# Optimization experiments

Measured on AMD Instinct MI355X. Metric: run time of the kernel, lower is better.

Reference implementation:

```python
import jax, jax.numpy as jnp
import numpy as np

D_MODEL = 2048
N_HEAD = 32
N_KV_HEAD = 8
HEAD_DIM = D_MODEL // N_HEAD  # 64
N_REP = N_HEAD // N_KV_HEAD   # 4
B, T = 2, 2048


def setup_inputs() -> dict:
    key = jax.random.key(0)
    ks = jax.random.split(key, 5)
    s = 0.02
    return {
        "x": jax.random.normal(ks[0], (B, T, D_MODEL), dtype=jnp.float32),
        "Wq": jax.random.normal(ks[1], (D_MODEL, N_HEAD * HEAD_DIM), dtype=jnp.float32) * s,
        "Wk": jax.random.normal(ks[2], (D_MODEL, N_KV_HEAD * HEAD_DIM), dtype=jnp.float32) * s,
        "Wv": jax.random.normal(ks[3], (D_MODEL, N_KV_HEAD * HEAD_DIM), dtype=jnp.float32) * s,
        "Wo": jax.random.normal(ks[4], (N_HEAD * HEAD_DIM, D_MODEL), dtype=jnp.float32) * s,
        "mask": 1,
    }


def _rope_tables(t_len, dim, dtype):
    inv_freq = 1.0 / (10000.0 ** (jnp.arange(0, dim, 2, dtype=jnp.float32) / dim))
    freqs = jnp.arange(t_len, dtype=jnp.float32)[:, None] * inv_freq[None, :]  # [T, dim/2]
    return jnp.cos(freqs).astype(dtype), jnp.sin(freqs).astype(dtype)


def _apply_rope(x, cos, sin):
    # x: [B, H, T, D]; cos/sin: [T, D/2]; half-concat layout as in source
    x1, x2 = x[..., ::2], x[..., 1::2]
    return jnp.concatenate([x1 * cos - x2 * sin, x1 * sin + x2 * cos], axis=-1)


def reference(x, Wq, Wk, Wv, Wo, mask):
    b, t, c = x.shape
    q = (x @ Wq).reshape(b, t, N_HEAD, HEAD_DIM).transpose(0, 2, 1, 3)      # [B,H,T,D]
    k = (x @ Wk).reshape(b, t, N_KV_HEAD, HEAD_DIM).transpose(0, 2, 1, 3)   # [B,Hkv,T,D]
    v = (x @ Wv).reshape(b, t, N_KV_HEAD, HEAD_DIM).transpose(0, 2, 1, 3)
    cos, sin = _rope_tables(t, HEAD_DIM, x.dtype)
    q = _apply_rope(q, cos, sin)
    k = _apply_rope(k, cos, sin)
    k = jnp.repeat(k, N_REP, axis=1)  # [B,H,T,D]
    v = jnp.repeat(v, N_REP, axis=1)
    scale = 1.0 / np.sqrt(HEAD_DIM)
    scores = jnp.einsum('bhtd,bhsd->bhts', q, k) * scale  # [B,H,T,T]
    if mask:
        causal = jnp.tril(jnp.ones((t, t), dtype=bool))
        scores = jnp.where(causal, scores, jnp.float32(-jnp.inf).astype(scores.dtype))
    weights = jax.nn.softmax(scores, axis=-1)
    out = jnp.einsum('bhts,bhsd->bhtd', weights, v)        # [B,H,T,D]
    out = out.transpose(0, 2, 1, 3).reshape(b, t, c)
    return out @ Wo
```

## Files before the change

kernel.cpp:

```cpp
#include <hip/hip_runtime.h>
#include <stdint.h>

#define D_MODEL 2048
#define N_HEAD 32
#define N_KV_HEAD 8
#define HEAD_DIM 64
#define BATCH 2
#define SEQ 2048
#define ROWS (BATCH*SEQ)
#define QKV_N 3072
#define SCL2F 0.18033688011112042f

typedef __attribute__((ext_vector_type(4))) float f32x4;
typedef __attribute__((ext_vector_type(8))) short bf16x8;

__device__ __forceinline__ float bflo(unsigned u){ return __uint_as_float(u << 16); }
__device__ __forceinline__ float bfhi(unsigned u){ return __uint_as_float(u & 0xFFFF0000u); }
__device__ __forceinline__ unsigned f2bf(float f){
  unsigned u = __float_as_uint(f);
  u += 0x7FFFu + ((u >> 16) & 1u);
  return u >> 16;
}
__device__ __forceinline__ unsigned cvtpk(float a, float b){
  unsigned r;
  asm("v_cvt_pk_bf16_f32 %0, %1, %2" : "=v"(r) : "v"(a), "v"(b));
  return r;
}

__device__ __forceinline__ void async_copy16(const void* g, void* lds){
  __builtin_amdgcn_global_load_lds(
      (const __attribute__((address_space(1))) void*)g,
      (__attribute__((address_space(3))) void*)lds, 16, 0, 0);
}

__global__ __launch_bounds__(256) void k_cvt_bf16(const float* __restrict__ in,
                                                  unsigned short* __restrict__ out, int n4){
  int i = blockIdx.x*256 + threadIdx.x;
  if (i >= n4) return;
  float4 v = ((const float4*)in)[i];
  unsigned lo = f2bf(v.x) | (f2bf(v.y) << 16);
  unsigned hi = f2bf(v.z) | (f2bf(v.w) << 16);
  ((uint2*)out)[i] = make_uint2(lo, hi);
}

__global__ __launch_bounds__(256) void k_transpose_all(const float* __restrict__ Wq,
                                                       const float* __restrict__ Wk,
                                                       const float* __restrict__ Wv,
                                                       const float* __restrict__ Wo,
                                                       unsigned short* __restrict__ Wqkvt,
                                                       unsigned short* __restrict__ Wot){
  const int bid = blockIdx.x;
  const float* W; unsigned short* Wt; int N; int rel;
  if (bid < 1024)      { W = Wq; Wt = Wqkvt;                         N = 2048; rel = bid; }
  else if (bid < 1280) { W = Wk; Wt = Wqkvt + (size_t)2048*D_MODEL;  N = 512;  rel = bid - 1024; }
  else if (bid < 1536) { W = Wv; Wt = Wqkvt + (size_t)2560*D_MODEL;  N = 512;  rel = bid - 1280; }
  else                 { W = Wo; Wt = Wot;                           N = 2048; rel = bid - 1536; }
  __shared__ float tile[64][65];
  const int ntn = N >> 6;
  const int tk = rel / ntn, tn = rel % ntn;
  const int tid = threadIdx.x;
  #pragma unroll
  for (int i = 0; i < 4; ++i) {
    int idx4 = tid + 256*i;
    int r = idx4 >> 4;
    int c4 = idx4 & 15;
    float4 v = *(const float4*)(W + (size_t)(tk*64 + r)*N + tn*64 + c4*4);
    tile[r][c4*4+0] = v.x; tile[r][c4*4+1] = v.y;
    tile[r][c4*4+2] = v.z; tile[r][c4*4+3] = v.w;
  }
  __syncthreads();
  #pragma unroll
  for (int i = 0; i < 8; ++i) {
    int o2 = tid + 256*i;
    int n  = o2 >> 5;
    int k2 = o2 & 31;
    unsigned lo = f2bf(tile[k2*2+0][n]);
    unsigned hi = f2bf(tile[k2*2+1][n]);
    *(unsigned*)(Wt + (size_t)(tn*64 + n)*D_MODEL + tk*64 + k2*2) = lo | (hi << 16);
  }
}

__global__ __launch_bounds__(256) void k_rope_tables(float* __restrict__ ct, float* __restrict__ st){
  int gid = blockIdx.x*256 + threadIdx.x;
  int t = gid >> 5, d = gid & 31;
  float inv = exp2f(-13.287712379549449f * ((float)d * (1.0f/32.0f)));
  float a = (float)t * inv;
  ct[gid] = cosf(a);
  st[gid] = sinf(a);
}

__global__ __launch_bounds__(256) void k_rope_apply(unsigned short* __restrict__ X,
                                                    const float* __restrict__ ct,
                                                    const float* __restrict__ st,
                                                    int nheads, int stride, float scale){
  int gid = blockIdx.x*256 + threadIdx.x;
  int row = gid / nheads;
  int h = gid - row*nheads;
  int t = row & (SEQ-1);
  unsigned* p = (unsigned*)(X + (size_t)row*stride + h*HEAD_DIM);
  float o1[32], o2[32];
  #pragma unroll
  for (int d = 0; d < 32; ++d) {
    unsigned u = p[d];
    float x1 = bflo(u), x2 = bfhi(u);
    float c = ct[t*32+d], s = st[t*32+d];
    o1[d] = (x1*c - x2*s)*scale;
    o2[d] = (x1*s + x2*c)*scale;
  }
  #pragma unroll
  for (int i = 0; i < 16; ++i) {
    p[i]    = f2bf(o1[2*i]) | (f2bf(o1[2*i+1]) << 16);
    p[16+i] = f2bf(o2[2*i]) | (f2bf(o2[2*i+1]) << 16);
  }
}

template<typename OUT_T>
__global__ __launch_bounds__(256) void k_gemm_bt(const unsigned short* __restrict__ A,
                                                 const unsigned short* __restrict__ Bt,
                                                 OUT_T* __restrict__ C,
                                                 int M, int N, int K){
  __shared__ unsigned short As[128*32];
  __shared__ unsigned short Bs[128*32];
  const int nbn = N >> 7;
  const int bm = blockIdx.x / nbn, bn = blockIdx.x % nbn;
  const int m0 = bm << 7, n0 = bn << 7;
  const int tid = threadIdx.x;
  const int wid = tid >> 6, lane = tid & 63;
  const int wr = wid >> 1, wc = wid & 1;

  f32x4 acc[4][4] = {};

  const int ldr = lane >> 2;
  const int ldc = (lane & 3) * 8;
  const int fr  = lane & 15;
  const int fk  = (lane >> 4) * 8;

  for (int k0 = 0; k0 < K; k0 += 32) {
    #pragma unroll
    for (int i = 0; i < 2; ++i) {
      int chunk = wid*2 + i;
      int row = chunk*16 + ldr;
      async_copy16(A  + (size_t)(m0+row)*K + k0 + ldc, (void*)(As + chunk*512));
      async_copy16(Bt + (size_t)(n0+row)*K + k0 + ldc, (void*)(Bs + chunk*512));
    }
    __syncthreads();
    bf16x8 a[4], b[4];
    #pragma unroll
    for (int m = 0; m < 4; ++m) a[m] = *(const bf16x8*)(As + (wr*64 + m*16 + fr)*32 + fk);
    #pragma unroll
    for (int n = 0; n < 4; ++n) b[n] = *(const bf16x8*)(Bs + (wc*64 + n*16 + fr)*32 + fk);
    #pragma unroll
    for (int m = 0; m < 4; ++m)
      #pragma unroll
      for (int n = 0; n < 4; ++n)
        acc[m][n] = __builtin_amdgcn_mfma_f32_16x16x32_bf16(a[m], b[n], acc[m][n], 0, 0, 0);
    __syncthreads();
  }

  const int crow = (lane >> 4) * 4, ccol = lane & 15;
  #pragma unroll
  for (int m = 0; m < 4; ++m){
    #pragma unroll
    for (int n = 0; n < 4; ++n){
      size_t base = (size_t)(m0 + wr*64 + m*16 + crow)*N + (n0 + wc*64 + n*16 + ccol);
      #pragma unroll
      for (int j = 0; j < 4; ++j){
        float v = acc[m][n][j];
        if constexpr (sizeof(OUT_T) == 2)
          ((unsigned short*)C)[base + (size_t)j*N] = (unsigned short)f2bf(v);
        else
          ((float*)C)[base + (size_t)j*N] = v;
      }
    }
  }
}

__global__ __launch_bounds__(256) void k_transpose_v(const unsigned short* __restrict__ Vsrc,
                                                     unsigned short* __restrict__ Vt, int stride){
  __shared__ __align__(16) unsigned short t[64*64];
  const int bk = blockIdx.x >> 5;
  const int st = blockIdx.x & 31;
  const int b = bk >> 3, kvh = bk & 7;
  const int tid = threadIdx.x;
  #pragma unroll
  for (int it = 0; it < 2; ++it) {
    int i = tid + 256*it;
    int s = i >> 3, c = i & 7;
    uint4 v = *(const uint4*)(Vsrc + (size_t)(b*SEQ + st*64 + s)*stride + kvh*HEAD_DIM + c*8);
    *(uint4*)(t + s*64 + ((c ^ (s&7))*8)) = v;
  }
  __syncthreads();
  const int d = tid & 63;
  const int w = tid >> 6;
  #pragma unroll
  for (int it = 0; it < 2; ++it) {
    int seg = w + it*4;
    unsigned short tmp[8];
    #pragma unroll
    for (int k = 0; k < 8; ++k) {
      int s = seg*8 + k;
      tmp[k] = t[s*64 + (((d>>3) ^ (s&7))*8) + (d&7)];
    }
    *(uint4*)(Vt + ((size_t)bk*64 + d)*SEQ + st*64 + seg*8) = *(uint4*)tmp;
  }
}

__global__ __launch_bounds__(256) void k_attn_mfma(const unsigned short* __restrict__ Q,
                                                   const unsigned short* __restrict__ Kb,
                                                   const unsigned short* __restrict__ Vt,
                                                   unsigned short* __restrict__ O,
                                                   const int* __restrict__ maskp,
                                                   const float* __restrict__ ct,
                                                   const float* __restrict__ st){
  __shared__ __align__(16) char smem[32768];
  char* Vsm = smem + 16384;
  const int orig = blockIdx.x;
  const int bid = (orig & 7)*128 + (orig >> 3);
  const int jj = bid & 15;
  const int h  = (bid >> 4) & 31;
  const int b  = bid >> 9;
  const int kvh = h >> 2;
  const int tid = threadIdx.x;
  const int wid = tid >> 6, lane = tid & 63;
  const int q_ = lane & 15, g = lane >> 4;
  char* Psm = smem + 24576 + wid*2048;
  const bool causal = (maskp[0] != 0);

  auto stageK = [&](int tile, int bufbase){
    const int s0s = tile*64;
    #pragma unroll
    for (int it = 0; it < 2; ++it) {
      int i = (wid*2+it)*64 + lane;
      int s = i >> 3, c = i & 7;
      async_copy16(Kb + (size_t)(b*SEQ + s0s + s)*QKV_N + kvh*HEAD_DIM + ((c ^ (s&7))*8),
                   smem + bufbase + (wid*2+it)*1024);
    }
  };
  auto stageV = [&](int tile){
    const int s0s = tile*64;
    #pragma unroll
    for (int it = 0; it < 2; ++it) {
      int i = (wid*2+it)*64 + lane;
      int s = i >> 3, c = i & 7;
      async_copy16(Vt + ((size_t)(b*N_KV_HEAD + kvh)*HEAD_DIM + s)*SEQ + s0s + ((c ^ (s&7))*8),
                   Vsm + (wid*2+it)*1024);
    }
  };

  for (int pass = 0; pass < 2; ++pass) {
    const int qt = pass ? jj : (31 - jj);
    const int q0 = qt*64;
    const int qg = q0 + 16*wid + q_;
    const int nt = causal ? (qt+1) : (SEQ/64);

    bf16x8 qf0, qf1;
    {
      const int trow = qg;
      const unsigned short* qsrc = Q + (size_t)(b*SEQ + trow)*QKV_N + h*HEAD_DIM + g*16;
      union { bf16x8 h; unsigned u[4]; } xa, xb;
      xa.h = *(const bf16x8*)(qsrc);
      xb.h = *(const bf16x8*)(qsrc + 8);
      const float4* cp = (const float4*)(ct + trow*32 + g*8);
      const float4* sp = (const float4*)(st + trow*32 + g*8);
      float4 c0 = cp[0], c1 = cp[1];
      float4 s0 = sp[0], s1 = sp[1];
      float cc[8] = {c0.x,c0.y,c0.z,c0.w,c1.x,c1.y,c1.z,c1.w};
      float ss[8] = {s0.x,s0.y,s0.z,s0.w,s1.x,s1.y,s1.z,s1.w};
      float e0[8], e1[8];
      #pragma unroll
      for (int e = 0; e < 8; ++e) {
        unsigned u = (e < 4) ? xa.u[e] : xb.u[e-4];
        float x1 = bflo(u), x2 = bfhi(u);
        float cs = cc[e]*SCL2F, sn = ss[e]*SCL2F;
        e0[e] = x1*cs - x2*sn;
        e1[e] = x1*sn + x2*cs;
      }
      union { unsigned u[4]; bf16x8 h; } p0, p1;
      #pragma unroll
      for (int m = 0; m < 4; ++m) {
        p0.u[m] = cvtpk(e0[2*m], e0[2*m+1]);
        p1.u[m] = cvtpk(e1[2*m], e1[2*m+1]);
      }
      qf0 = p0.h; qf1 = p1.h;
    }

    f32x4 acc[4] = {};
    float mrun = -1e30f, lrun = 0.f;

    stageK(0, 0);
    stageV(0);
    asm volatile("s_waitcnt vmcnt(0)" ::: "memory");
    __syncthreads();

    for (int t = 0; t < nt; ++t) {
      const int s0 = t*64;
      const int cur = t & 1;
      const char* Kbuf = smem + cur*8192;

      if (t+1 < nt) stageK(t+1, (cur^1)*8192);

      f32x4 sa[4];
      __builtin_amdgcn_s_setprio(1);
      #pragma unroll
      for (int f = 0; f < 4; ++f) {
        const char* kb = Kbuf + (16*f + q_)*128;
        bf16x8 a0 = *(const bf16x8*)(kb + ((g ^ (q_&7))*16));
        bf16x8 a1 = *(const bf16x8*)(kb + (((g+4) ^ (q_&7))*16));
        f32x4 z = {};
        z = __builtin_amdgcn_mfma_f32_16x16x32_bf16(a0, qf0, z, 0, 0, 0);
        z = __builtin_amdgcn_mfma_f32_16x16x32_bf16(a1, qf1, z, 0, 0, 0);
        sa[f] = z;
      }
      __builtin_amdgcn_s_setprio(0);

      const bool domask = causal && (t == qt);
      float x[4][4];
      float cm[4];
      #pragma unroll
      for (int f = 0; f < 4; ++f) {
        #pragma unroll
        for (int r = 0; r < 4; ++r) {
          float v = sa[f][r];
          if (domask && (s0 + 16*f + 4*g + r > qg)) v = -3.0e38f;
          x[f][r] = v;
        }
        cm[f] = fmaxf(fmaxf(x[f][0], x[f][1]), fmaxf(x[f][2], x[f][3]));
      }
      float cmax = fmaxf(fmaxf(cm[0], cm[1]), fmaxf(cm[2], cm[3]));
      cmax = fmaxf(cmax, __shfl_xor(cmax, 16));
      cmax = fmaxf(cmax, __shfl_xor(cmax, 32));
      if (!__all(cmax <= mrun + 8.0f)) {
        float mnew = fmaxf(mrun, cmax);
        float r2 = exp2f(mrun - mnew);
        lrun *= r2;
        #pragma unroll
        for (int m = 0; m < 4; ++m) {
          acc[m][0] *= r2; acc[m][1] *= r2; acc[m][2] *= r2; acc[m][3] *= r2;
        }
        mrun = mnew;
      }
      float sf[4];
      #pragma unroll
      for (int f = 0; f < 4; ++f) {
        float e0 = exp2f(x[f][0] - mrun);
        float e1 = exp2f(x[f][1] - mrun);
        float e2 = exp2f(x[f][2] - mrun);
        float e3 = exp2f(x[f][3] - mrun);
        sf[f] = (e0 + e1) + (e2 + e3);
        uint2 w = { cvtpk(e0, e1), cvtpk(e2, e3) };
        int byteo = q_*128 + (((2*f + (g>>1)) ^ (q_&7))*16) + (g&1)*8;
        *(uint2*)(Psm + byteo) = w;
      }
      float tsum = (sf[0] + sf[1]) + (sf[2] + sf[3]);
      tsum += __shfl_xor(tsum, 16);
      tsum += __shfl_xor(tsum, 32);
      lrun += tsum;

      asm volatile("s_waitcnt vmcnt(0)" ::: "memory");
      __syncthreads();

      __builtin_amdgcn_s_setprio(1);
      #pragma unroll
      for (int kh = 0; kh < 2; ++kh) {
        bf16x8 pb = *(const bf16x8*)(Psm + q_*128 + (((g + 4*kh) ^ (q_&7))*16));
        #pragma unroll
        for (int m = 0; m < 4; ++m) {
          bf16x8 va = *(const bf16x8*)(Vsm + (16*m + q_)*128 + (((g + 4*kh) ^ (q_&7))*16));
          acc[m] = __builtin_amdgcn_mfma_f32_16x16x32_bf16(va, pb, acc[m], 0, 0, 0);
        }
      }
      __builtin_amdgcn_s_setprio(0);

      __syncthreads();
      if (t+1 < nt) stageV(t+1);
    }

    float inv = 1.0f / lrun;
    #pragma unroll
    for (int m = 0; m < 4; ++m) {
      uint2 w = { cvtpk(acc[m][0]*inv, acc[m][1]*inv), cvtpk(acc[m][2]*inv, acc[m][3]*inv) };
      int byteo = q_*128 + (((2*m + (g>>1)) ^ (q_&7))*16) + (g&1)*8;
      *(uint2*)(Psm + byteo) = w;
    }
    #pragma unroll
    for (int cc = 0; cc < 2; ++cc) {
      int row = lane >> 2;
      int ch = (lane & 3)*2 + cc;
      uint4 v = *(const uint4*)(Psm + row*128 + ((ch ^ (row&7))*16));
      *(uint4*)(O + (size_t)(b*SEQ + q0 + 16*wid + row)*D_MODEL + h*HEAD_DIM + ch*8) = v;
    }
  }
}

extern "C" void kernel_launch(void* const* d_in, const int* in_sizes, int n_in,
                              void* d_out, int out_size, void* d_ws, size_t ws_size,
                              hipStream_t stream){
  const float* x  = (const float*)d_in[0];
  const float* Wq = (const float*)d_in[1];
  const float* Wk = (const float*)d_in[2];
  const float* Wv = (const float*)d_in[3];
  const float* Wo = (const float*)d_in[4];
  const int* maskp = (const int*)d_in[5];
  float* out = (float*)d_out;

  char* ws = (char*)d_ws;
  unsigned short* xb    = (unsigned short*)(ws);
  unsigned short* AO    = (unsigned short*)(ws);
  unsigned short* Wqkvt = (unsigned short*)(ws + 16777216);
  unsigned short* Vt    = (unsigned short*)(ws + 16777216);
  unsigned short* Wot   = (unsigned short*)(ws + 29360128);
  unsigned short* QKVb  = (unsigned short*)(ws + 37748736);
  float* ct = (float*)(ws + 62914560);
  float* st = (float*)(ws + 63176704);

  k_cvt_bf16<<<8192, 256, 0, stream>>>(x, xb, ROWS*D_MODEL/4);
  k_transpose_all<<<2560, 256, 0, stream>>>(Wq, Wk, Wv, Wo, Wqkvt, Wot);
  k_rope_tables<<<SEQ*32/256, 256, 0, stream>>>(ct, st);

  k_gemm_bt<unsigned short><<<(4096/128)*(QKV_N/128), 256, 0, stream>>>(xb, Wqkvt, QKVb, 4096, QKV_N, 2048);

  k_rope_apply<<<ROWS*N_KV_HEAD/256, 256, 0, stream>>>(QKVb + 2048, ct, st, N_KV_HEAD, QKV_N, 1.0f);

  k_transpose_v<<<BATCH*N_KV_HEAD*(SEQ/64), 256, 0, stream>>>(QKVb + 2560, Vt, QKV_N);

  k_attn_mfma<<<BATCH*N_HEAD*16, 256, 0, stream>>>(QKVb, QKVb + 2048, Vt, AO, maskp, ct, st);

  k_gemm_bt<float><<<(4096/128)*(2048/128), 256, 0, stream>>>(AO, Wot, out, 4096, 2048, 2048);
}
```

Before: 247.5 us.

## Merge prep kernels, swizzle GEMM block order, compute softmax denominator via MFMA

Folds the input conversion, weight transposes and RoPE table kernels into one launch to cut launch overhead and tail idle time. Remaps GEMM block indices so that consecutive blocks land on different XCDs, aiming for better L2 locality. In attention, replaces the per-tile exp-sum and cross-lane shuffles with an extra MFMA against a ones vector that accumulates the row sum in bf16-rounded form. This adds one MFMA per k-half and makes the denominator use the same bf16-rounded probabilities as the numerator.

```diff
diff --git a/kernel.cpp b/kernel.cpp
--- a/kernel.cpp
+++ b/kernel.cpp
@@ -33,60 +33,65 @@
       (__attribute__((address_space(3))) void*)lds, 16, 0, 0);
 }
 
-__global__ __launch_bounds__(256) void k_cvt_bf16(const float* __restrict__ in,
-                                                  unsigned short* __restrict__ out, int n4){
-  int i = blockIdx.x*256 + threadIdx.x;
-  if (i >= n4) return;
-  float4 v = ((const float4*)in)[i];
-  unsigned lo = f2bf(v.x) | (f2bf(v.y) << 16);
-  unsigned hi = f2bf(v.z) | (f2bf(v.w) << 16);
-  ((uint2*)out)[i] = make_uint2(lo, hi);
-}
-
-__global__ __launch_bounds__(256) void k_transpose_all(const float* __restrict__ Wq,
-                                                       const float* __restrict__ Wk,
-                                                       const float* __restrict__ Wv,
-                                                       const float* __restrict__ Wo,
-                                                       unsigned short* __restrict__ Wqkvt,
-                                                       unsigned short* __restrict__ Wot){
+__global__ __launch_bounds__(256) void k_prep(const float* __restrict__ x,
+                                              const float* __restrict__ Wq,
+                                              const float* __restrict__ Wk,
+                                              const float* __restrict__ Wv,
+                                              const float* __restrict__ Wo,
+                                              unsigned short* __restrict__ xb,
+                                              unsigned short* __restrict__ Wqkvt,
+                                              unsigned short* __restrict__ Wot,
+                                              float* __restrict__ ct,
+                                              float* __restrict__ st){
+  __shared__ float tile[64][65];
   const int bid = blockIdx.x;
-  const float* W; unsigned short* Wt; int N; int rel;
-  if (bid < 1024)      { W = Wq; Wt = Wqkvt;                         N = 2048; rel = bid; }
-  else if (bid < 1280) { W = Wk; Wt = Wqkvt + (size_t)2048*D_MODEL;  N = 512;  rel = bid - 1024; }
-  else if (bid < 1536) { W = Wv; Wt = Wqkvt + (size_t)2560*D_MODEL;  N = 512;  rel = bid - 1280; }
-  else                 { W = Wo; Wt = Wot;                           N = 2048; rel = bid - 1536; }
-  __shared__ float tile[64][65];
-  const int ntn = N >> 6;
-  const int tk = rel / ntn, tn = rel % ntn;
   const int tid = threadIdx.x;
-  #pragma unroll
-  for (int i = 0; i < 4; ++i) {
-    int idx4 = tid + 256*i;
-    int r = idx4 >> 4;
-    int c4 = idx4 & 15;
-    float4 v = *(const float4*)(W + (size_t)(tk*64 + r)*N + tn*64 + c4*4);
-    tile[r][c4*4+0] = v.x; tile[r][c4*4+1] = v.y;
-    tile[r][c4*4+2] = v.z; tile[r][c4*4+3] = v.w;
-  }
-  __syncthreads();
-  #pragma unroll
-  for (int i = 0; i < 8; ++i) {
-    int o2 = tid + 256*i;
-    int n  = o2 >> 5;
-    int k2 = o2 & 31;
-    unsigned lo = f2bf(tile[k2*2+0][n]);
-    unsigned hi = f2bf(tile[k2*2+1][n]);
-    *(unsigned*)(Wt + (size_t)(tn*64 + n)*D_MODEL + tk*64 + k2*2) = lo | (hi << 16);
-  }
-}
-
-__global__ __launch_bounds__(256) void k_rope_tables(float* __restrict__ ct, float* __restrict__ st){
-  int gid = blockIdx.x*256 + threadIdx.x;
-  int t = gid >> 5, d = gid & 31;
-  float inv = exp2f(-13.287712379549449f * ((float)d * (1.0f/32.0f)));
-  float a = (float)t * inv;
-  ct[gid] = cosf(a);
-  st[gid] = sinf(a);
+  if (bid < 8192) {
+    int i = bid*256 + tid;
+    float4 v = ((const float4*)x)[i];
+    unsigned lo = f2bf(v.x) | (f2bf(v.y) << 16);
+    unsigned hi = f2bf(v.z) | (f2bf(v.w) << 16);
+    ((uint2*)xb)[i] = make_uint2(lo, hi);
+    return;
+  }
+  if (bid < 10752) {
+    const int rel0 = bid - 8192;
+    const float* W; unsigned short* Wt; int N; int rel;
+    if (rel0 < 1024)      { W = Wq; Wt = Wqkvt;                         N = 2048; rel = rel0; }
+    else if (rel0 < 1280) { W = Wk; Wt = Wqkvt + (size_t)2048*D_MODEL;  N = 512;  rel = rel0 - 1024; }
+    else if (rel0 < 1536) { W = Wv; Wt = Wqkvt + (size_t)2560*D_MODEL;  N = 512;  rel = rel0 - 1280; }
+    else                  { W = Wo; Wt = Wot;                           N = 2048; rel = rel0 - 1536; }
+    const int ntn = N >> 6;
+    const int tk = rel / ntn, tn = rel % ntn;
+    #pragma unroll
+    for (int i = 0; i < 4; ++i) {
+      int idx4 = tid + 256*i;
+      int r = idx4 >> 4;
+      int c4 = idx4 & 15;
+      float4 v = *(const float4*)(W + (size_t)(tk*64 + r)*N + tn*64 + c4*4);
+      tile[r][c4*4+0] = v.x; tile[r][c4*4+1] = v.y;
+      tile[r][c4*4+2] = v.z; tile[r][c4*4+3] = v.w;
+    }
+    __syncthreads();
+    #pragma unroll
+    for (int i = 0; i < 8; ++i) {
+      int o2 = tid + 256*i;
+      int n  = o2 >> 5;
+      int k2 = o2 & 31;
+      unsigned lo = f2bf(tile[k2*2+0][n]);
+      unsigned hi = f2bf(tile[k2*2+1][n]);
+      *(unsigned*)(Wt + (size_t)(tn*64 + n)*D_MODEL + tk*64 + k2*2) = lo | (hi << 16);
+    }
+    return;
+  }
+  {
+    int gid = (bid - 10752)*256 + tid;
+    int t = gid >> 5, d = gid & 31;
+    float inv = exp2f(-13.287712379549449f * ((float)d * (1.0f/32.0f)));
+    float a = (float)t * inv;
+    ct[gid] = cosf(a);
+    st[gid] = sinf(a);
+  }
 }
 
 __global__ __launch_bounds__(256) void k_rope_apply(unsigned short* __restrict__ X,
@@ -122,7 +127,8 @@
   __shared__ unsigned short As[128*32];
   __shared__ unsigned short Bs[128*32];
   const int nbn = N >> 7;
-  const int bm = blockIdx.x / nbn, bn = blockIdx.x % nbn;
+  const int bswz = ((int)blockIdx.x & 7)*((int)gridDim.x >> 3) + ((int)blockIdx.x >> 3);
+  const int bm = bswz / nbn, bn = bswz % nbn;
   const int m0 = bm << 7, n0 = bn << 7;
   const int tid = threadIdx.x;
   const int wid = tid >> 6, lane = tid & 63;
@@ -226,6 +232,10 @@
   char* Psm = smem + 24576 + wid*2048;
   const bool causal = (maskp[0] != 0);
 
+  bf16x8 onesf;
+  #pragma unroll
+  for (int e = 0; e < 8; ++e) onesf[e] = (short)0x3F80;
+
   auto stageK = [&](int tile, int bufbase){
     const int s0s = tile*64;
     #pragma unroll
@@ -285,7 +295,8 @@
     }
 
     f32x4 acc[4] = {};
-    float mrun = -1e30f, lrun = 0.f;
+    f32x4 accl = {};
+    float mrun = -1e30f;
 
     stageK(0, 0);
     stageV(0);
@@ -332,29 +343,23 @@
       if (!__all(cmax <= mrun + 8.0f)) {
         float mnew = fmaxf(mrun, cmax);
         float r2 = exp2f(mrun - mnew);
-        lrun *= r2;
         #pragma unroll
         for (int m = 0; m < 4; ++m) {
           acc[m][0] *= r2; acc[m][1] *= r2; acc[m][2] *= r2; acc[m][3] *= r2;
         }
+        accl[0] *= r2; accl[1] *= r2; accl[2] *= r2; accl[3] *= r2;
         mrun = mnew;
       }
-      float sf[4];
       #pragma unroll
       for (int f = 0; f < 4; ++f) {
         float e0 = exp2f(x[f][0] - mrun);
         float e1 = exp2f(x[f][1] - mrun);
         float e2 = exp2f(x[f][2] - mrun);
         float e3 = exp2f(x[f][3] - mrun);
-        sf[f] = (e0 + e1) + (e2 + e3);
         uint2 w = { cvtpk(e0, e1), cvtpk(e2, e3) };
         int byteo = q_*128 + (((2*f + (g>>1)) ^ (q_&7))*16) + (g&1)*8;
         *(uint2*)(Psm + byteo) = w;
       }
-      float tsum = (sf[0] + sf[1]) + (sf[2] + sf[3]);
-      tsum += __shfl_xor(tsum, 16);
-      tsum += __shfl_xor(tsum, 32);
-      lrun += tsum;
 
       asm volatile("s_waitcnt vmcnt(0)" ::: "memory");
       __syncthreads();
@@ -363,6 +368,7 @@
       #pragma unroll
       for (int kh = 0; kh < 2; ++kh) {
         bf16x8 pb = *(const bf16x8*)(Psm + q_*128 + (((g + 4*kh) ^ (q_&7))*16));
+        accl = __builtin_amdgcn_mfma_f32_16x16x32_bf16(onesf, pb, accl, 0, 0, 0);
         #pragma unroll
         for (int m = 0; m < 4; ++m) {
           bf16x8 va = *(const bf16x8*)(Vsm + (16*m + q_)*128 + (((g + 4*kh) ^ (q_&7))*16));
@@ -375,7 +381,7 @@
       if (t+1 < nt) stageV(t+1);
     }
 
-    float inv = 1.0f / lrun;
+    float inv = 1.0f / accl[0];
     #pragma unroll
     for (int m = 0; m < 4; ++m) {
       uint2 w = { cvtpk(acc[m][0]*inv, acc[m][1]*inv), cvtpk(acc[m][2]*inv, acc[m][3]*inv) };
@@ -413,9 +419,7 @@
   float* ct = (float*)(ws + 62914560);
   float* st = (float*)(ws + 63176704);
 
-  k_cvt_bf16<<<8192, 256, 0, stream>>>(x, xb, ROWS*D_MODEL/4);
-  k_transpose_all<<<2560, 256, 0, stream>>>(Wq, Wk, Wv, Wo, Wqkvt, Wot);
-  k_rope_tables<<<SEQ*32/256, 256, 0, stream>>>(ct, st);
+  k_prep<<<11008, 256, 0, stream>>>(x, Wq, Wk, Wv, Wo, xb, Wqkvt, Wot, ct, st);
 
   k_gemm_bt<unsigned short><<<(4096/128)*(QKV_N/128), 256, 0, stream>>>(xb, Wqkvt, QKVb, 4096, QKV_N, 2048);
 
```

Result: faster. 240.5 us (-2.8%).
